# Performance work log

Hardware: AMD Instinct MI355X
Metric: run time of the kernel (lower is better)

Reference implementation:

```python
import jax, jax.numpy as jnp
from jax import lax
import numpy as np

D = 256        # input_size / hidden_dim
NRELS = 8      # rel_types hard-coded in WeightedGNN
V = 50257      # ntokens
PAD = 0        # padding_idx
L = 64         # max sequence length
B = 16         # batch size


def layer_norm(x, eps=1e-5):
    # F.layer_norm with no affine params
    m = jnp.mean(x, axis=-1, keepdims=True)
    v = jnp.var(x, axis=-1, keepdims=True)
    return (x - m) * lax.rsqrt(v + eps)


def setup_inputs() -> dict:
    key = jax.random.key(0)
    ks = jax.random.split(key, 10)
    tokens = jax.random.randint(ks[0], (L, B), 0, V)            # [L, B] like torch input
    A_rels = jax.random.uniform(ks[1], (B, L, L, NRELS), dtype=jnp.float32)
    root = jax.random.uniform(ks[2], (B, L), dtype=jnp.float32)
    s = 1.0 / np.sqrt(D)
    emb_sem = (jax.random.normal(ks[3], (V, D), jnp.float32) * 0.02).at[PAD].set(0.0)
    W_proj_nbrs = jax.random.normal(ks[4], (D, NRELS * D), jnp.float32) * s
    b_proj_nbrs = jnp.zeros((NRELS * D,), jnp.float32)
    W_in = jax.random.normal(ks[5], (D, 3 * D), jnp.float32) * s
    b_in = jnp.zeros((3 * D,), jnp.float32)
    W_out = jax.random.normal(ks[6], (D, D), jnp.float32) * s
    b_out = jnp.zeros((D,), jnp.float32)
    return dict(tokens=tokens, A_rels=A_rels, root=root, emb_sem=emb_sem,
                W_proj_nbrs=W_proj_nbrs, b_proj_nbrs=b_proj_nbrs,
                W_in=W_in, b_in=b_in, W_out=W_out, b_out=b_out)


def reference(tokens, A_rels, root, emb_sem, W_proj_nbrs, b_proj_nbrs, W_in, b_in, W_out, b_out):
    tok = tokens.T                                  # [B, L]
    mask = tok != PAD                               # [B, L]
    lengths = mask.sum(axis=1)                      # [B]
    X_sem = emb_sem[tok]                            # [B, L, D] (pad row is zero)

    # in_proj(x) is identical every iteration (dropout is eval-mode identity) -> hoist
    shift, scale, proj_x = jnp.split(X_sem @ W_in + b_in, 3, axis=-1)  # each [B, L, D]

    def step(h_prev, i):
        # relation-typed neighbor projection + per-relation layer norm
        p = (h_prev @ W_proj_nbrs + b_proj_nbrs).reshape(B, L, NRELS, D)
        p = layer_norm(p)
        # weighted aggregation over source nodes i and relation types h
        lin_sum = jnp.einsum('bijh,bihd->bjd', A_rels, p)          # [B, L, D]
        shr = lin_sum - jnp.tanh(lin_sum)                          # shrink()
        h = jax.nn.relu(shift * layer_norm(proj_x + shr) + scale)  # gated update
        y = jnp.tanh(h @ W_out + b_out)
        y = jnp.where((i > lengths)[:, None, None], 0.0, y)        # masked_fill
        return y, None

    prev0 = jnp.zeros_like(X_sem)
    prev_level, _ = lax.scan(step, prev0, jnp.arange(L, 0, -1))    # i = L..1
    final_state = jnp.einsum('bih,bi->bh', prev_level, root)       # [B, D]
    return final_state
```

## Files before the change

### kernel.cpp

```cpp
#include <hip/hip_runtime.h>
#include <hip/hip_bf16.h>


#define DD 256
#define LLEN 64
#define BBAT 16
#define NROWS 1024

typedef __attribute__((ext_vector_type(8))) short short8;
typedef __attribute__((ext_vector_type(4))) float f32x4;

__device__ inline unsigned short f2bf(float x) {
    unsigned int u = __float_as_uint(x);
    unsigned int r = (u + 0x7fffu + ((u >> 16) & 1u)) >> 16;
    return (unsigned short)r;
}

__global__ void k_setup(const int* __restrict__ tokens, int* __restrict__ lengths) {
    int b = threadIdx.x;
    if (b < BBAT) {
        int c = 0;
        for (int l = 0; l < LLEN; ++l) c += (tokens[l * BBAT + b] != 0) ? 1 : 0;
        lengths[b] = c;
    }
}

__global__ __launch_bounds__(256) void k_cvtW(const float* __restrict__ Wp,
                                              unsigned short* __restrict__ Wf) {
    int t = blockIdx.x * 256 + threadIdx.x;
    int l = t & 63; int rest = t >> 6;
    int tk = rest & 7; rest >>= 3;
    int tn = rest & 15; int hh = rest >> 4;
    int kbase = tk * 32 + (l >> 4) * 8;
    int n = hh * 256 + tn * 16 + (l & 15);
    union { short8 v; unsigned short u[8]; } pk;
#pragma unroll
    for (int j = 0; j < 8; ++j) pk.u[j] = f2bf(Wp[(kbase + j) * 2048 + n]);
    *(short8*)(Wf + (long)t * 8) = pk.v;
}

__global__ __launch_bounds__(256) void k_cvtA(const float* __restrict__ A,
                                              unsigned short* __restrict__ Af) {
    int t = blockIdx.x * 256 + threadIdx.x;
    int lane = t & 63;
    int tk = (t >> 6) & 15;
    int jg = (t >> 10) & 3;
    int b  = t >> 12;
    int j = jg * 16 + (lane & 15);
    int kbase = tk * 32 + (lane >> 4) * 8;
    int h  = kbase >> 6;
    int i0 = kbase & 63;
    union { short8 v; unsigned short u[8]; } pk;
#pragma unroll
    for (int jj = 0; jj < 8; ++jj)
        pk.u[jj] = f2bf(A[((long)(b * 64 + i0 + jj) * 64 + j) * 8 + h]);
    *(short8*)(Af + (long)t * 8) = pk.v;
}

__global__ __launch_bounds__(256) void k_cvtWo(const float* __restrict__ Wo,
                                               unsigned short* __restrict__ Wof) {
    int t = blockIdx.x * 256 + threadIdx.x;
    int lane = t & 63;
    int tk = (t >> 6) & 7;
    int nt = t >> 9;
    int kbase = tk * 32 + (lane >> 4) * 8;
    int n = nt * 16 + (lane & 15);
    union { short8 v; unsigned short u[8]; } pk;
#pragma unroll
    for (int j = 0; j < 8; ++j) pk.u[j] = f2bf(Wo[(kbase + j) * 256 + n]);
    *(short8*)(Wof + (long)t * 8) = pk.v;
}

__global__ __launch_bounds__(256) void k_inproj(
    const int* __restrict__ tokens, const float* __restrict__ emb,
    const float* __restrict__ W_in, const float* __restrict__ b_in,
    float* __restrict__ shiftb, float* __restrict__ scaleb, float* __restrict__ projx)
{
    __shared__ float xs[8][DD];
    const int t = threadIdx.x;
    const int row0 = blockIdx.x * 8;
    for (int r = 0; r < 8; ++r) {
        int row = row0 + r;
        int b = row >> 6, l = row & 63;
        int tok = tokens[l * BBAT + b];
        xs[r][t] = emb[(long)tok * DD + t];
    }
    __syncthreads();
    float a0[8], a1[8], a2[8];
#pragma unroll
    for (int r = 0; r < 8; ++r) { a0[r] = a1[r] = a2[r] = 0.f; }
    for (int k = 0; k < DD; ++k) {
        float w0 = W_in[k * 768 + t];
        float w1 = W_in[k * 768 + 256 + t];
        float w2 = W_in[k * 768 + 512 + t];
#pragma unroll
        for (int r = 0; r < 8; ++r) {
            float x = xs[r][k];
            a0[r] = fmaf(x, w0, a0[r]);
            a1[r] = fmaf(x, w1, a1[r]);
            a2[r] = fmaf(x, w2, a2[r]);
        }
    }
    float bi0 = b_in[t], bi1 = b_in[256 + t], bi2 = b_in[512 + t];
#pragma unroll
    for (int r = 0; r < 8; ++r) {
        int row = row0 + r;
        shiftb[row * DD + t] = a0[r] + bi0;
        scaleb[row * DD + t] = a1[r] + bi1;
        projx [row * DD + t] = a2[r] + bi2;
    }
}

__global__ __launch_bounds__(256, 2) void k_proj(
    const unsigned short* __restrict__ h_bf,
    const unsigned short* __restrict__ Wf,
    const float* __restrict__ bp,
    unsigned short* __restrict__ Pf)
{
    __shared__ float Cs[16][260];
    __shared__ float part[4][16][2];
    const int t = threadIdx.x;
    const int wv = t >> 6, lane = t & 63;
    const int lin = blockIdx.x;
    const int xcd = lin & 7, q = lin >> 3;
    const int b = xcd + 8 * (q & 1);
    const int rest = q >> 1;
    const int hh = rest & 7;
    const int ig = rest >> 3;
    const int row0 = b * 64 + ig * 16;

    f32x4 acc[4];
#pragma unroll
    for (int tn = 0; tn < 4; ++tn) acc[tn] = (f32x4){0.f, 0.f, 0.f, 0.f};

    const unsigned short* aRow = h_bf + (row0 + (lane & 15)) * DD + (lane >> 4) * 8;
    const unsigned short* wBase = Wf + ((long)(hh * 16 + wv * 4) * 8) * 512 + lane * 8;
    short8 a8[8];
#pragma unroll
    for (int tk = 0; tk < 8; ++tk) a8[tk] = *(const short8*)(aRow + tk * 32);
#pragma unroll
    for (int tk = 0; tk < 8; ++tk) {
#pragma unroll
        for (int tn = 0; tn < 4; ++tn) {
            short8 bb = *(const short8*)(wBase + (long)(tn * 8 + tk) * 512);
            acc[tn] = __builtin_amdgcn_mfma_f32_16x16x32_bf16(a8[tk], bb, acc[tn], 0, 0, 0);
        }
    }
#pragma unroll
    for (int tn = 0; tn < 4; ++tn) {
        int n = wv * 64 + tn * 16 + (lane & 15);
        int m0 = (lane >> 4) * 4;
#pragma unroll
        for (int r = 0; r < 4; ++r) Cs[m0 + r][n] = acc[tn][r];
    }
    __syncthreads();
    const float bias = bp[hh * 256 + t];
    float vals[16];
#pragma unroll
    for (int r = 0; r < 16; ++r) vals[r] = Cs[r][t] + bias;
    for (int r = 0; r < 16; ++r) {
        float s = vals[r], ss = vals[r] * vals[r];
#pragma unroll
        for (int m = 32; m >= 1; m >>= 1) { s += __shfl_xor(s, m); ss += __shfl_xor(ss, m); }
        if (lane == 0) { part[wv][r][0] = s; part[wv][r][1] = ss; }
    }
    __syncthreads();
    float normed[16];
#pragma unroll
    for (int r = 0; r < 16; ++r) {
        float s  = part[0][r][0] + part[1][r][0] + part[2][r][0] + part[3][r][0];
        float ss = part[0][r][1] + part[1][r][1] + part[2][r][1] + part[3][r][1];
        float mean = s * (1.f / 256.f);
        float var  = ss * (1.f / 256.f) - mean * mean;
        float rstd = rsqrtf(var + 1e-5f);
        normed[r] = (vals[r] - mean) * rstd;
    }
    const int ibase = ig * 16;
#pragma unroll
    for (int g = 0; g < 2; ++g) {
        int k0 = hh * 64 + ibase + g * 8;
        int tk1 = k0 >> 5;
        int lane_s = ((k0 >> 3) & 3) * 16 + (t & 15);
        long off = (long)b * 131072 + tk1 * 8192 + (t >> 4) * 512 + lane_s * 8;
        union { short8 v; unsigned short u[8]; } pk;
#pragma unroll
        for (int jj = 0; jj < 8; ++jj) pk.u[jj] = f2bf(normed[g * 8 + jj]);
        *(short8*)(Pf + off) = pk.v;
    }
}

__global__ __launch_bounds__(1024) void k_agg(
    const unsigned short* __restrict__ Af,
    const unsigned short* __restrict__ Pf,
    const float* __restrict__ projx,
    const float* __restrict__ shiftb,
    const float* __restrict__ scaleb,
    const unsigned short* __restrict__ Wof,
    const float* __restrict__ bout,
    const int* __restrict__ lengths,
    float* __restrict__ h_out,
    unsigned short* __restrict__ h_bf,
    int i_val, int write_f32)
{
    __shared__ float Cs[16][260];
    __shared__ unsigned short hsb[16][264];
    __shared__ float part[16][4][2];
    const int t = threadIdx.x;
    const int w = t >> 6, lane = t & 63;
    const int b = blockIdx.x, jg = blockIdx.y;
    const int j0 = jg * 16;

    const unsigned short* ab = Af + ((long)(b * 4 + jg) * 16) * 512 + lane * 8;
    const unsigned short* pb = Pf + (long)b * 131072 + w * 512 + lane * 8;
    short8 bfr[16];
#pragma unroll
    for (int tk = 0; tk < 16; ++tk)
        bfr[tk] = *(const short8*)(pb + (long)tk * 8192);
    f32x4 acc = (f32x4){0.f, 0.f, 0.f, 0.f};
#pragma unroll
    for (int tk = 0; tk < 16; ++tk) {
        short8 a = *(const short8*)(ab + (long)tk * 512);
        acc = __builtin_amdgcn_mfma_f32_16x16x32_bf16(a, bfr[tk], acc, 0, 0, 0);
    }
    {
        int n = w * 16 + (lane & 15);
        int m0 = (lane >> 4) * 4;
#pragma unroll
        for (int r = 0; r < 4; ++r) Cs[m0 + r][n] = acc[r];
    }
    __syncthreads();

    const int d = t & 255;
    const int rbase = (w >> 2) * 4;
    const int dseg = w & 3;
    float tv[4];
#pragma unroll
    for (int ri = 0; ri < 4; ++ri) {
        int row = b * 64 + j0 + rbase + ri;
        float lin = Cs[rbase + ri][d];
        float shr = lin - tanhf(lin);
        tv[ri] = projx[row * DD + d] + shr;
    }
#pragma unroll
    for (int ri = 0; ri < 4; ++ri) {
        float s = tv[ri], ss = tv[ri] * tv[ri];
#pragma unroll
        for (int m = 32; m >= 1; m >>= 1) { s += __shfl_xor(s, m); ss += __shfl_xor(ss, m); }
        if (lane == 0) { part[rbase + ri][dseg][0] = s; part[rbase + ri][dseg][1] = ss; }
    }
    __syncthreads();
#pragma unroll
    for (int ri = 0; ri < 4; ++ri) {
        int r = rbase + ri;
        int row = b * 64 + j0 + r;
        float s  = part[r][0][0] + part[r][1][0] + part[r][2][0] + part[r][3][0];
        float ss = part[r][0][1] + part[r][1][1] + part[r][2][1] + part[r][3][1];
        float mean = s * (1.f / 256.f);
        float var  = ss * (1.f / 256.f) - mean * mean;
        float rstd = rsqrtf(var + 1e-5f);
        float nv = (tv[ri] - mean) * rstd;
        float hv = fmaf(shiftb[row * DD + d], nv, scaleb[row * DD + d]);
        hsb[r][d] = f2bf(fmaxf(hv, 0.f));
    }
    __syncthreads();

    f32x4 acc2 = (f32x4){0.f, 0.f, 0.f, 0.f};
#pragma unroll
    for (int tk = 0; tk < 8; ++tk) {
        short8 a = *(const short8*)(&hsb[lane & 15][tk * 32 + (lane >> 4) * 8]);
        short8 wf = *(const short8*)(Wof + (long)(w * 8 + tk) * 512 + lane * 8);
        acc2 = __builtin_amdgcn_mfma_f32_16x16x32_bf16(a, wf, acc2, 0, 0, 0);
    }
    {
        int n = w * 16 + (lane & 15);
        int m0 = (lane >> 4) * 4;
#pragma unroll
        for (int r = 0; r < 4; ++r) Cs[m0 + r][n] = acc2[r];
    }
    __syncthreads();
    const float bo_d = bout[d];
    const bool maskz = (i_val > lengths[b]);
#pragma unroll
    for (int ri = 0; ri < 4; ++ri) {
        int r = rbase + ri;
        int row = b * 64 + j0 + r;
        float y = tanhf(Cs[r][d] + bo_d);
        float ym = maskz ? 0.f : y;
        h_bf[row * DD + d] = f2bf(ym);
        if (write_f32) h_out[row * DD + d] = ym;
    }
}

__global__ __launch_bounds__(256) void k_final(
    const float* __restrict__ h_buf, const float* __restrict__ root,
    float* __restrict__ out)
{
    const int t = threadIdx.x;
    const int b = blockIdx.x;
    float acc = 0.f;
    for (int i = 0; i < LLEN; ++i)
        acc = fmaf(h_buf[(b * 64 + i) * DD + t], root[b * 64 + i], acc);
    out[b * DD + t] = acc;
}

extern "C" void kernel_launch(void* const* d_in, const int* in_sizes, int n_in,
                              void* d_out, int out_size, void* d_ws, size_t ws_size,
                              hipStream_t stream)
{
    const int*   tokens = (const int*)  d_in[0];
    const float* A      = (const float*)d_in[1];
    const float* root   = (const float*)d_in[2];
    const float* emb    = (const float*)d_in[3];
    const float* Wp     = (const float*)d_in[4];
    const float* bp     = (const float*)d_in[5];
    const float* Wi     = (const float*)d_in[6];
    const float* bi     = (const float*)d_in[7];
    const float* Wo     = (const float*)d_in[8];
    const float* bo     = (const float*)d_in[9];
    float* out = (float*)d_out;

    char* ws = (char*)d_ws;
    int*   lengths = (int*)(ws + 0);
    float* shiftb  = (float*)(ws + 1024);
    float* scaleb  = shiftb + NROWS * DD;
    float* projx   = scaleb + NROWS * DD;
    float* h_out   = projx  + NROWS * DD;
    unsigned short* h_bf = (unsigned short*)(h_out + NROWS * DD);
    unsigned short* Wf   = h_bf + NROWS * DD;
    unsigned short* Pf   = Wf + 524288;
    unsigned short* Af   = Pf + 2097152;
    unsigned short* Wof  = Af + 524288;

    hipMemsetAsync(h_bf, 0, (size_t)NROWS * DD * sizeof(unsigned short), stream);
    k_setup<<<1, 64, 0, stream>>>(tokens, lengths);
    k_cvtW<<<256, 256, 0, stream>>>(Wp, Wf);
    k_cvtA<<<256, 256, 0, stream>>>(A, Af);
    k_cvtWo<<<32, 256, 0, stream>>>(Wo, Wof);
    k_inproj<<<128, 256, 0, stream>>>(tokens, emb, Wi, bi, shiftb, scaleb, projx);
    for (int it = 0; it < 64; ++it) {
        int i_val = 64 - it;
        k_proj<<<512, 256, 0, stream>>>(h_bf, Wf, bp, Pf);
        k_agg<<<dim3(16, 4), 1024, 0, stream>>>(Af, Pf, projx, shiftb, scaleb,
                                                Wof, bo, lengths, h_out, h_bf,
                                                i_val, (it == 63) ? 1 : 0);
    }
    k_final<<<16, 256, 0, stream>>>(h_out, root, out);
}
```

Measured before the change: 1.586 ms.

## Fuse recurrent loop into persistent kernel with per-batch atomic barriers

Replaces the 128 per-step kernel launches (projection + aggregation) and the final reduction with one persistent kernel of 64 blocks. The blocks for each batch element synchronise through a global atomic counter barrier. The projection layer-norm now reduces inside each wave group. Lengths and the final root-weighted sum are folded into the same kernel. This removes launch overhead and inter-kernel gaps, but relies on all 64 blocks being co-resident and adds spin-wait barrier latency.

```diff
diff --git a/kernel.cpp b/kernel.cpp
--- a/kernel.cpp
+++ b/kernel.cpp
@@ -8,6 +8,7 @@
 #define NROWS 1024
 
 typedef __attribute__((ext_vector_type(8))) short short8;
+typedef __attribute__((ext_vector_type(4))) short short4v;
 typedef __attribute__((ext_vector_type(4))) float f32x4;
 
 __device__ inline unsigned short f2bf(float x) {
@@ -16,13 +17,16 @@
     return (unsigned short)r;
 }
 
-__global__ void k_setup(const int* __restrict__ tokens, int* __restrict__ lengths) {
-    int b = threadIdx.x;
-    if (b < BBAT) {
-        int c = 0;
-        for (int l = 0; l < LLEN; ++l) c += (tokens[l * BBAT + b] != 0) ? 1 : 0;
-        lengths[b] = c;
-    }
+__device__ inline void b_bar(int* barp, int target, int t) {
+    __syncthreads();
+    if (t == 0) {
+        __threadfence();
+        __hip_atomic_fetch_add(barp, 1, __ATOMIC_RELAXED, __HIP_MEMORY_SCOPE_AGENT);
+        while (__hip_atomic_load(barp, __ATOMIC_RELAXED, __HIP_MEMORY_SCOPE_AGENT) < target)
+            __builtin_amdgcn_s_sleep(2);
+        __threadfence();
+    }
+    __syncthreads();
 }
 
 __global__ __launch_bounds__(256) void k_cvtW(const float* __restrict__ Wp,
@@ -111,196 +115,219 @@
     }
 }
 
-__global__ __launch_bounds__(256, 2) void k_proj(
-    const unsigned short* __restrict__ h_bf,
+__global__ __launch_bounds__(1024) void k_fused(
+    const int* __restrict__ tokens,
+    const unsigned short* __restrict__ Af,
     const unsigned short* __restrict__ Wf,
+    const unsigned short* __restrict__ Wof,
     const float* __restrict__ bp,
-    unsigned short* __restrict__ Pf)
-{
-    __shared__ float Cs[16][260];
-    __shared__ float part[4][16][2];
-    const int t = threadIdx.x;
-    const int wv = t >> 6, lane = t & 63;
-    const int lin = blockIdx.x;
-    const int xcd = lin & 7, q = lin >> 3;
-    const int b = xcd + 8 * (q & 1);
-    const int rest = q >> 1;
-    const int hh = rest & 7;
-    const int ig = rest >> 3;
-    const int row0 = b * 64 + ig * 16;
-
-    f32x4 acc[4];
-#pragma unroll
-    for (int tn = 0; tn < 4; ++tn) acc[tn] = (f32x4){0.f, 0.f, 0.f, 0.f};
-
-    const unsigned short* aRow = h_bf + (row0 + (lane & 15)) * DD + (lane >> 4) * 8;
-    const unsigned short* wBase = Wf + ((long)(hh * 16 + wv * 4) * 8) * 512 + lane * 8;
-    short8 a8[8];
-#pragma unroll
-    for (int tk = 0; tk < 8; ++tk) a8[tk] = *(const short8*)(aRow + tk * 32);
-#pragma unroll
-    for (int tk = 0; tk < 8; ++tk) {
-#pragma unroll
-        for (int tn = 0; tn < 4; ++tn) {
-            short8 bb = *(const short8*)(wBase + (long)(tn * 8 + tk) * 512);
-            acc[tn] = __builtin_amdgcn_mfma_f32_16x16x32_bf16(a8[tk], bb, acc[tn], 0, 0, 0);
-        }
-    }
-#pragma unroll
-    for (int tn = 0; tn < 4; ++tn) {
-        int n = wv * 64 + tn * 16 + (lane & 15);
-        int m0 = (lane >> 4) * 4;
-#pragma unroll
-        for (int r = 0; r < 4; ++r) Cs[m0 + r][n] = acc[tn][r];
-    }
-    __syncthreads();
-    const float bias = bp[hh * 256 + t];
-    float vals[16];
-#pragma unroll
-    for (int r = 0; r < 16; ++r) vals[r] = Cs[r][t] + bias;
-    for (int r = 0; r < 16; ++r) {
-        float s = vals[r], ss = vals[r] * vals[r];
-#pragma unroll
-        for (int m = 32; m >= 1; m >>= 1) { s += __shfl_xor(s, m); ss += __shfl_xor(ss, m); }
-        if (lane == 0) { part[wv][r][0] = s; part[wv][r][1] = ss; }
-    }
-    __syncthreads();
-    float normed[16];
-#pragma unroll
-    for (int r = 0; r < 16; ++r) {
-        float s  = part[0][r][0] + part[1][r][0] + part[2][r][0] + part[3][r][0];
-        float ss = part[0][r][1] + part[1][r][1] + part[2][r][1] + part[3][r][1];
-        float mean = s * (1.f / 256.f);
-        float var  = ss * (1.f / 256.f) - mean * mean;
-        float rstd = rsqrtf(var + 1e-5f);
-        normed[r] = (vals[r] - mean) * rstd;
-    }
-    const int ibase = ig * 16;
-#pragma unroll
-    for (int g = 0; g < 2; ++g) {
-        int k0 = hh * 64 + ibase + g * 8;
-        int tk1 = k0 >> 5;
-        int lane_s = ((k0 >> 3) & 3) * 16 + (t & 15);
-        long off = (long)b * 131072 + tk1 * 8192 + (t >> 4) * 512 + lane_s * 8;
-        union { short8 v; unsigned short u[8]; } pk;
-#pragma unroll
-        for (int jj = 0; jj < 8; ++jj) pk.u[jj] = f2bf(normed[g * 8 + jj]);
-        *(short8*)(Pf + off) = pk.v;
-    }
-}
-
-__global__ __launch_bounds__(1024) void k_agg(
-    const unsigned short* __restrict__ Af,
-    const unsigned short* __restrict__ Pf,
+    const float* __restrict__ bout,
     const float* __restrict__ projx,
     const float* __restrict__ shiftb,
     const float* __restrict__ scaleb,
-    const unsigned short* __restrict__ Wof,
-    const float* __restrict__ bout,
-    const int* __restrict__ lengths,
+    const float* __restrict__ root,
+    unsigned short* __restrict__ h_bf,
+    unsigned short* __restrict__ Pf,
     float* __restrict__ h_out,
-    unsigned short* __restrict__ h_bf,
-    int i_val, int write_f32)
+    float* __restrict__ out,
+    int* __restrict__ bars)
 {
-    __shared__ float Cs[16][260];
+    __shared__ float p1part[4][2][4][16][2];
+    __shared__ float Cs2[16][260];
     __shared__ unsigned short hsb[16][264];
-    __shared__ float part[16][4][2];
+    __shared__ float part2[16][4][2];
+    __shared__ int len_s;
+
     const int t = threadIdx.x;
-    const int w = t >> 6, lane = t & 63;
-    const int b = blockIdx.x, jg = blockIdx.y;
-    const int j0 = jg * 16;
-
-    const unsigned short* ab = Af + ((long)(b * 4 + jg) * 16) * 512 + lane * 8;
-    const unsigned short* pb = Pf + (long)b * 131072 + w * 512 + lane * 8;
-    short8 bfr[16];
-#pragma unroll
-    for (int tk = 0; tk < 16; ++tk)
-        bfr[tk] = *(const short8*)(pb + (long)tk * 8192);
-    f32x4 acc = (f32x4){0.f, 0.f, 0.f, 0.f};
-#pragma unroll
-    for (int tk = 0; tk < 16; ++tk) {
-        short8 a = *(const short8*)(ab + (long)tk * 512);
-        acc = __builtin_amdgcn_mfma_f32_16x16x32_bf16(a, bfr[tk], acc, 0, 0, 0);
-    }
-    {
-        int n = w * 16 + (lane & 15);
-        int m0 = (lane >> 4) * 4;
-#pragma unroll
-        for (int r = 0; r < 4; ++r) Cs[m0 + r][n] = acc[r];
+    const int lane = t & 63;
+    const int q = lane >> 4;
+    const int blk = blockIdx.x;
+    const int b = (blk & 7) + 8 * ((blk >> 3) & 1);
+    const int s16 = blk >> 4;
+    const int sub = t >> 8;
+    const int wv = (t >> 6) & 3;
+    const int w = t >> 6;
+
+    if (t < 64) {
+        int tok = tokens[t * BBAT + b];
+        unsigned long long m = __ballot(tok != 0);
+        if (t == 0) len_s = __popcll(m);
     }
     __syncthreads();
 
-    const int d = t & 255;
-    const int rbase = (w >> 2) * 4;
-    const int dseg = w & 3;
-    float tv[4];
-#pragma unroll
-    for (int ri = 0; ri < 4; ++ri) {
-        int row = b * 64 + j0 + rbase + ri;
-        float lin = Cs[rbase + ri][d];
-        float shr = lin - tanhf(lin);
-        tv[ri] = projx[row * DD + d] + shr;
-    }
-#pragma unroll
-    for (int ri = 0; ri < 4; ++ri) {
-        float s = tv[ri], ss = tv[ri] * tv[ri];
-#pragma unroll
-        for (int m = 32; m >= 1; m >>= 1) { s += __shfl_xor(s, m); ss += __shfl_xor(ss, m); }
-        if (lane == 0) { part[rbase + ri][dseg][0] = s; part[rbase + ri][dseg][1] = ss; }
-    }
-    __syncthreads();
-#pragma unroll
-    for (int ri = 0; ri < 4; ++ri) {
-        int r = rbase + ri;
-        int row = b * 64 + j0 + r;
-        float s  = part[r][0][0] + part[r][1][0] + part[r][2][0] + part[r][3][0];
-        float ss = part[r][0][1] + part[r][1][1] + part[r][2][1] + part[r][3][1];
-        float mean = s * (1.f / 256.f);
-        float var  = ss * (1.f / 256.f) - mean * mean;
-        float rstd = rsqrtf(var + 1e-5f);
-        float nv = (tv[ri] - mean) * rstd;
-        float hv = fmaf(shiftb[row * DD + d], nv, scaleb[row * DD + d]);
-        hsb[r][d] = f2bf(fmaxf(hv, 0.f));
-    }
-    __syncthreads();
-
-    f32x4 acc2 = (f32x4){0.f, 0.f, 0.f, 0.f};
-#pragma unroll
-    for (int tk = 0; tk < 8; ++tk) {
-        short8 a = *(const short8*)(&hsb[lane & 15][tk * 32 + (lane >> 4) * 8]);
-        short8 wf = *(const short8*)(Wof + (long)(w * 8 + tk) * 512 + lane * 8);
-        acc2 = __builtin_amdgcn_mfma_f32_16x16x32_bf16(a, wf, acc2, 0, 0, 0);
-    }
-    {
-        int n = w * 16 + (lane & 15);
-        int m0 = (lane >> 4) * 4;
-#pragma unroll
-        for (int r = 0; r < 4; ++r) Cs[m0 + r][n] = acc2[r];
-    }
-    __syncthreads();
-    const float bo_d = bout[d];
-    const bool maskz = (i_val > lengths[b]);
-#pragma unroll
-    for (int ri = 0; ri < 4; ++ri) {
-        int r = rbase + ri;
-        int row = b * 64 + j0 + r;
-        float y = tanhf(Cs[r][d] + bo_d);
-        float ym = maskz ? 0.f : y;
-        h_bf[row * DD + d] = f2bf(ym);
-        if (write_f32) h_out[row * DD + d] = ym;
-    }
-}
-
-__global__ __launch_bounds__(256) void k_final(
-    const float* __restrict__ h_buf, const float* __restrict__ root,
-    float* __restrict__ out)
-{
-    const int t = threadIdx.x;
-    const int b = blockIdx.x;
-    float acc = 0.f;
-    for (int i = 0; i < LLEN; ++i)
-        acc = fmaf(h_buf[(b * 64 + i) * DD + t], root[b * 64 + i], acc);
-    out[b * DD + t] = acc;
+    int* barp = bars + b * 32;
+    int barcnt = 0;
+    const int row0 = b * 64 + s16 * 16;
+    const int j0 = s16 * 16;
+
+    for (int it = 0; it < 64; ++it) {
+#pragma unroll
+        for (int uu = 0; uu < 2; ++uu) {
+            const int hh = sub * 2 + uu;
+            f32x4 acc[4];
+#pragma unroll
+            for (int tn = 0; tn < 4; ++tn) acc[tn] = (f32x4){0.f, 0.f, 0.f, 0.f};
+            const unsigned short* aRow = h_bf + (row0 + (lane & 15)) * DD + q * 8;
+            const unsigned short* wBase = Wf + ((long)(hh * 16 + wv * 4) * 8) * 512 + lane * 8;
+            short8 a8[8];
+#pragma unroll
+            for (int tk = 0; tk < 8; ++tk) a8[tk] = *(const short8*)(aRow + tk * 32);
+#pragma unroll
+            for (int tk = 0; tk < 8; ++tk) {
+#pragma unroll
+                for (int tn = 0; tn < 4; ++tn) {
+                    short8 bb = *(const short8*)(wBase + (long)(tn * 8 + tk) * 512);
+                    acc[tn] = __builtin_amdgcn_mfma_f32_16x16x32_bf16(a8[tk], bb, acc[tn], 0, 0, 0);
+                }
+            }
+            float bpv[4];
+#pragma unroll
+            for (int tn = 0; tn < 4; ++tn)
+                bpv[tn] = bp[hh * 256 + wv * 64 + tn * 16 + (lane & 15)];
+            float v[4][4], s[4], ss[4];
+#pragma unroll
+            for (int r = 0; r < 4; ++r) {
+                s[r] = 0.f; ss[r] = 0.f;
+#pragma unroll
+                for (int tn = 0; tn < 4; ++tn) {
+                    float x = acc[tn][r] + bpv[tn];
+                    v[tn][r] = x;
+                    s[r] += x; ss[r] += x * x;
+                }
+#pragma unroll
+                for (int msk = 1; msk < 16; msk <<= 1) {
+                    s[r]  += __shfl_xor(s[r],  msk);
+                    ss[r] += __shfl_xor(ss[r], msk);
+                }
+            }
+            if ((lane & 15) == 0) {
+#pragma unroll
+                for (int r = 0; r < 4; ++r) {
+                    p1part[sub][uu][wv][q * 4 + r][0] = s[r];
+                    p1part[sub][uu][wv][q * 4 + r][1] = ss[r];
+                }
+            }
+            __syncthreads();
+            float mean[4], rstd[4];
+#pragma unroll
+            for (int r = 0; r < 4; ++r) {
+                int mrow = q * 4 + r;
+                float S  = p1part[sub][uu][0][mrow][0] + p1part[sub][uu][1][mrow][0]
+                         + p1part[sub][uu][2][mrow][0] + p1part[sub][uu][3][mrow][0];
+                float SS = p1part[sub][uu][0][mrow][1] + p1part[sub][uu][1][mrow][1]
+                         + p1part[sub][uu][2][mrow][1] + p1part[sub][uu][3][mrow][1];
+                float mn = S * (1.f / 256.f);
+                float var = SS * (1.f / 256.f) - mn * mn;
+                mean[r] = mn;
+                rstd[r] = rsqrtf(var + 1e-5f);
+            }
+            const int kbase = hh * 64 + s16 * 16 + q * 4;
+            const int tk1 = kbase >> 5;
+            const int rowsel = (kbase >> 3) & 3;
+            const int jlo = (q & 1) * 4;
+#pragma unroll
+            for (int tn = 0; tn < 4; ++tn) {
+                short4v pk;
+#pragma unroll
+                for (int r = 0; r < 4; ++r)
+                    pk[r] = (short)f2bf((v[tn][r] - mean[r]) * rstd[r]);
+                long off = (long)b * 131072 + (long)tk1 * 8192 + (wv * 4 + tn) * 512
+                         + (rowsel * 16 + (lane & 15)) * 8 + jlo;
+                *(short4v*)(Pf + off) = pk;
+            }
+        }
+        ++barcnt; b_bar(barp, barcnt * 4, t);
+
+        {
+            const unsigned short* ab = Af + ((long)(b * 4 + s16) * 16) * 512 + lane * 8;
+            const unsigned short* pb = Pf + (long)b * 131072 + w * 512 + lane * 8;
+            short8 bfr[16];
+#pragma unroll
+            for (int tk = 0; tk < 16; ++tk) bfr[tk] = *(const short8*)(pb + (long)tk * 8192);
+            f32x4 acg = (f32x4){0.f, 0.f, 0.f, 0.f};
+#pragma unroll
+            for (int tk = 0; tk < 16; ++tk) {
+                short8 a = *(const short8*)(ab + (long)tk * 512);
+                acg = __builtin_amdgcn_mfma_f32_16x16x32_bf16(a, bfr[tk], acg, 0, 0, 0);
+            }
+            {
+                int n = w * 16 + (lane & 15);
+                int m0 = q * 4;
+#pragma unroll
+                for (int r = 0; r < 4; ++r) Cs2[m0 + r][n] = acg[r];
+            }
+            __syncthreads();
+            const int d = t & 255;
+            const int rbase = (w >> 2) * 4;
+            const int dseg = w & 3;
+            float tv[4];
+#pragma unroll
+            for (int ri = 0; ri < 4; ++ri) {
+                int row = b * 64 + j0 + rbase + ri;
+                float lin = Cs2[rbase + ri][d];
+                float shr = lin - tanhf(lin);
+                tv[ri] = projx[row * DD + d] + shr;
+            }
+#pragma unroll
+            for (int ri = 0; ri < 4; ++ri) {
+                float sv = tv[ri], sq = tv[ri] * tv[ri];
+#pragma unroll
+                for (int msk = 32; msk >= 1; msk >>= 1) {
+                    sv += __shfl_xor(sv, msk);
+                    sq += __shfl_xor(sq, msk);
+                }
+                if (lane == 0) { part2[rbase + ri][dseg][0] = sv; part2[rbase + ri][dseg][1] = sq; }
+            }
+            __syncthreads();
+#pragma unroll
+            for (int ri = 0; ri < 4; ++ri) {
+                int r = rbase + ri;
+                int row = b * 64 + j0 + r;
+                float S  = part2[r][0][0] + part2[r][1][0] + part2[r][2][0] + part2[r][3][0];
+                float SS = part2[r][0][1] + part2[r][1][1] + part2[r][2][1] + part2[r][3][1];
+                float mn = S * (1.f / 256.f);
+                float var = SS * (1.f / 256.f) - mn * mn;
+                float rs = rsqrtf(var + 1e-5f);
+                float nv = (tv[ri] - mn) * rs;
+                float hv = fmaf(shiftb[row * DD + d], nv, scaleb[row * DD + d]);
+                hsb[r][d] = f2bf(fmaxf(hv, 0.f));
+            }
+            __syncthreads();
+            f32x4 ac2 = (f32x4){0.f, 0.f, 0.f, 0.f};
+#pragma unroll
+            for (int tk = 0; tk < 8; ++tk) {
+                short8 a = *(const short8*)(&hsb[lane & 15][tk * 32 + q * 8]);
+                short8 wf = *(const short8*)(Wof + (long)(w * 8 + tk) * 512 + lane * 8);
+                ac2 = __builtin_amdgcn_mfma_f32_16x16x32_bf16(a, wf, ac2, 0, 0, 0);
+            }
+            {
+                int n = w * 16 + (lane & 15);
+                int m0 = q * 4;
+#pragma unroll
+                for (int r = 0; r < 4; ++r) Cs2[m0 + r][n] = ac2[r];
+            }
+            __syncthreads();
+            const float bo_d = bout[d];
+            const bool maskz = ((64 - it) > len_s);
+#pragma unroll
+            for (int ri = 0; ri < 4; ++ri) {
+                int r = rbase + ri;
+                int row = b * 64 + j0 + r;
+                float y = tanhf(Cs2[r][d] + bo_d);
+                float ym = maskz ? 0.f : y;
+                h_bf[row * DD + d] = f2bf(ym);
+                if (it == 63) h_out[row * DD + d] = ym;
+            }
+        }
+        ++barcnt; b_bar(barp, barcnt * 4, t);
+    }
+
+    if (s16 == 0 && t < 256) {
+        float accf = 0.f;
+        for (int i2 = 0; i2 < 64; ++i2)
+            accf = fmaf(h_out[(b * 64 + i2) * DD + t], root[b * 64 + i2], accf);
+        out[b * DD + t] = accf;
+    }
 }
 
 extern "C" void kernel_launch(void* const* d_in, const int* in_sizes, int n_in,
@@ -320,8 +347,8 @@
     float* out = (float*)d_out;
 
     char* ws = (char*)d_ws;
-    int*   lengths = (int*)(ws + 0);
-    float* shiftb  = (float*)(ws + 1024);
+    int*   bars    = (int*)(ws + 0);
+    float* shiftb  = (float*)(ws + 4096);
     float* scaleb  = shiftb + NROWS * DD;
     float* projx   = scaleb + NROWS * DD;
     float* h_out   = projx  + NROWS * DD;
@@ -331,18 +358,12 @@
     unsigned short* Af   = Pf + 2097152;
     unsigned short* Wof  = Af + 524288;
 
+    hipMemsetAsync(bars, 0, 4096, stream);
     hipMemsetAsync(h_bf, 0, (size_t)NROWS * DD * sizeof(unsigned short), stream);
-    k_setup<<<1, 64, 0, stream>>>(tokens, lengths);
     k_cvtW<<<256, 256, 0, stream>>>(Wp, Wf);
     k_cvtA<<<256, 256, 0, stream>>>(A, Af);
     k_cvtWo<<<32, 256, 0, stream>>>(Wo, Wof);
     k_inproj<<<128, 256, 0, stream>>>(tokens, emb, Wi, bi, shiftb, scaleb, projx);
-    for (int it = 0; it < 64; ++it) {
-        int i_val = 64 - it;
-        k_proj<<<512, 256, 0, stream>>>(h_bf, Wf, bp, Pf);
-        k_agg<<<dim3(16, 4), 1024, 0, stream>>>(Af, Pf, projx, shiftb, scaleb,
-                                                Wof, bo, lengths, h_out, h_bf,
-                                                i_val, (it == 63) ? 1 : 0);
-    }
-    k_final<<<16, 256, 0, stream>>>(h_out, root, out);
-}
+    k_fused<<<64, 1024, 0, stream>>>(tokens, Af, Wf, Wof, bp, bo, projx, shiftb, scaleb,
+                                     root, h_bf, Pf, h_out, out, bars);
+}
```

Result: slower. 4.304 ms (+171.3%).
